# Optimization experiments

Measured on AMD Instinct MI355X. Metric: run time of the kernel, lower is better.

## Reference

```python
import jax, jax.numpy as jnp
import numpy as np
from jax import lax

# ---- static config (matches init_kwargs) ----
B, CIN, COUT, WDIM = 16, 256, 3, 512
IN_SIZE, SR, IMG = 128, 128, 256
UP = IMG // SR                      # 2
CLAMP = 256.0
PAD_SIZE = (SR - IN_SIZE) * UP // 2  # 0


def _design_lowpass_filter(numtaps, cutoff, width, fs):
    """numpy reimplementation of scipy.signal.firwin (kaiser window, pass_zero)."""
    nyq = fs / 2.0
    # kaiser_atten / kaiser_beta
    atten = 2.285 * (numtaps - 1) * np.pi * (width / nyq) + 7.95
    if atten > 50:
        beta = 0.1102 * (atten - 8.7)
    elif atten > 21:
        beta = 0.5842 * (atten - 21) ** 0.4 + 0.07886 * (atten - 21)
    else:
        beta = 0.0
    m = np.arange(numtaps) - (numtaps - 1) / 2.0
    c = cutoff / nyq
    h = c * np.sinc(c * m)          # ideal lowpass
    h *= np.kaiser(numtaps, beta)   # kaiser window
    h /= h.sum()                    # unity DC gain (pass_zero scaling)
    return h.astype(np.float32)


def _upsample2d(x, f, up):
    """Faithful upfirdn2d.upsample2d: zero-insert upsample + separable FIR, gain=up^2."""
    C = x.shape[1]
    fw = f.shape[0]
    f = f * (up * up) ** 0.5        # sqrt(gain) per separable pass
    f = f[::-1]                     # flip (torch conv2d is correlation on flipped f)
    p0 = (fw + up - 1) // 2
    p1 = (fw - up) // 2 + (up - 1)  # +up-1: trailing zeros from zero-insertion
    dn = ('NCHW', 'OIHW', 'NCHW')
    kx = jnp.tile(f.reshape(1, 1, 1, fw), (C, 1, 1, 1))
    x = lax.conv_general_dilated(x, kx, window_strides=(1, 1),
                                 padding=((0, 0), (p0, p1)), lhs_dilation=(1, up),
                                 dimension_numbers=dn, feature_group_count=C)
    ky = jnp.tile(f.reshape(1, 1, fw, 1), (C, 1, 1, 1))
    x = lax.conv_general_dilated(x, ky, window_strides=(1, 1),
                                 padding=((p0, p1), (0, 0)), lhs_dilation=(up, 1),
                                 dimension_numbers=dn, feature_group_count=C)
    return x


def setup_inputs() -> dict:
    key = jax.random.key(0)
    k1, k2, k3, k4, k5 = jax.random.split(key, 5)
    up_filter = jnp.asarray(_design_lowpass_filter(
        numtaps=6 * UP + 1, cutoff=SR * 2 ** (-0.9), width=SR - SR * 2 ** (-0.9), fs=IMG))
    return {
        'x': jax.random.normal(k1, (B, CIN, IN_SIZE, IN_SIZE), jnp.float32),
        'w': jax.random.normal(k2, (B, WDIM), jnp.float32),
        'affine_weight': jax.random.normal(k3, (CIN, WDIM), jnp.float32),
        'affine_bias': jnp.ones((CIN,), jnp.float32),
        'conv_weight': jax.random.normal(k4, (COUT, CIN, 1, 1), jnp.float32),
        'conv_bias': jax.random.normal(k5, (COUT,), jnp.float32) * 0.1,
        'up_filter': up_filter,
    }


def reference(x, w, affine_weight, affine_bias, conv_weight, conv_bias, up_filter):
    # affine: FullyConnectedLayer (linear, weight_gain = 1/sqrt(w_dim)), then * 1/sqrt(in_ch*k^2)
    styles = (w @ (affine_weight.T * (1.0 / np.sqrt(WDIM))) + affine_bias) * (1.0 / np.sqrt(CIN))
    # modulated 1x1 grouped conv (demodulate=False): out[b,o] = sum_i W[o,i]*s[b,i]*x[b,i]
    k = conv_weight[:, :, 0, 0]                       # [COUT, CIN]
    y = jnp.einsum('bihw,oi,bi->bohw', x, k, styles)  # [B, COUT, H, W]
    # bias_act: bias + clamp
    y = jnp.clip(y + conv_bias.reshape(1, -1, 1, 1), -CLAMP, CLAMP)
    # FIR upsample (up_factor != 1) + pad (pad_size == 0 here)
    y = _upsample2d(y, up_filter, UP)
    if PAD_SIZE:
        y = jnp.pad(y, ((0, 0), (0, 0), (PAD_SIZE, PAD_SIZE), (PAD_SIZE, PAD_SIZE)))
    return y  # [B, COUT, IMG, IMG]
```

## Files before the change

kernel.cpp:

```cpp
#include <hip/hip_runtime.h>
#include <hip/hip_bf16.h>

#define B_    16
#define CIN_  256
#define COUT_ 3
#define WDIM_ 512
#define H_    128
#define HW_   (H_*H_)
#define OH_   256

__global__ __launch_bounds__(64) void k_styles(const float* __restrict__ w,
    const float* __restrict__ aw, const float* __restrict__ ab,
    const float* __restrict__ cw, float* __restrict__ mw)
{
    int bi = blockIdx.x;
    int b = bi >> 8, i = bi & 255;
    int lane = threadIdx.x;
    const float* wr = w + b * WDIM_;
    const float* ar = aw + (size_t)i * WDIM_;
    float s = 0.f;
    #pragma unroll
    for (int t = 0; t < 8; ++t) s += wr[lane + 64*t] * ar[lane + 64*t];
    #pragma unroll
    for (int off = 32; off > 0; off >>= 1) s += __shfl_down(s, off);
    if (lane == 0) {
        float st = (s * 0.04419417382415922f + ab[i]) * 0.0625f;
        float4 v;
        v.x = cw[i]          * st;
        v.y = cw[CIN_ + i]   * st;
        v.z = cw[2*CIN_ + i] * st;
        v.w = 0.f;
        reinterpret_cast<float4*>(mw)[bi] = v;
    }
}

__global__ __launch_bounds__(256) void k_conv(const float* __restrict__ x,
    const float* __restrict__ mw, const float* __restrict__ cb,
    float* __restrict__ y)
{
    int b    = blockIdx.x >> 5;
    int base = ((blockIdx.x & 31) << 9) + (threadIdx.x << 1);
    const float2* xp  = reinterpret_cast<const float2*>(x + (size_t)b * CIN_ * HW_ + base);
    const float4* mwp = reinterpret_cast<const float4*>(mw) + b * CIN_;
    float a0x=0.f,a0y=0.f,a1x=0.f,a1y=0.f,a2x=0.f,a2y=0.f;
    #pragma unroll 8
    for (int i = 0; i < CIN_; ++i) {
        float2 xv = xp[(size_t)i * (HW_/2)];
        float4 m  = mwp[i];
        a0x += xv.x*m.x; a0y += xv.y*m.x;
        a1x += xv.x*m.y; a1y += xv.y*m.y;
        a2x += xv.x*m.z; a2y += xv.y*m.z;
    }
    float b0 = cb[0], b1 = cb[1], b2 = cb[2];
    auto cl = [](float v){ return fminf(fmaxf(v, -256.f), 256.f); };
    float* yp = y + (size_t)b * COUT_ * HW_ + base;
    *reinterpret_cast<float2*>(yp)          = make_float2(cl(a0x+b0), cl(a0y+b0));
    *reinterpret_cast<float2*>(yp +   HW_)  = make_float2(cl(a1x+b1), cl(a1y+b1));
    *reinterpret_cast<float2*>(yp + 2*HW_)  = make_float2(cl(a2x+b2), cl(a2y+b2));
}

__global__ __launch_bounds__(256) void k_upx(const float* __restrict__ y,
    const float* __restrict__ f, float* __restrict__ t)
{
    int idx = blockIdx.x * 256 + threadIdx.x;
    int q   = idx & 127;
    int row = idx >> 7;
    const float* yr = y + (size_t)row * H_;
    int i0 = q - 3;
    float v[7];
    #pragma unroll
    for (int j = 0; j < 7; ++j) {
        int i = i0 + j;
        v[j] = (i >= 0 && i < H_) ? yr[i] : 0.f;
    }
    float e = 0.f, o = 0.f;
    #pragma unroll
    for (int j = 0; j < 6; ++j) e += v[j] * f[11 - 2*j];
    #pragma unroll
    for (int j = 0; j < 7; ++j) o += v[j] * f[12 - 2*j];
    reinterpret_cast<float2*>(t + (size_t)row * OH_)[q] = make_float2(e * 2.f, o * 2.f);
}

__global__ __launch_bounds__(256) void k_upy(const float* __restrict__ t,
    const float* __restrict__ f, float* __restrict__ out)
{
    int idx  = blockIdx.x * 256 + threadIdx.x;
    int qx   = idx & 127;
    int rest = idx >> 7;
    int qy   = rest & 127;
    int p    = rest >> 7;
    const float2* tc = reinterpret_cast<const float2*>(t + (size_t)p * H_ * OH_) + qx;
    int i0 = qy - 3;
    float2 v[7];
    #pragma unroll
    for (int j = 0; j < 7; ++j) {
        int i = i0 + j;
        v[j] = (i >= 0 && i < H_) ? tc[(size_t)i * (OH_/2)] : make_float2(0.f, 0.f);
    }
    float r0c0=0.f, r0c1=0.f, r1c0=0.f, r1c1=0.f;
    #pragma unroll
    for (int j = 0; j < 6; ++j) { float c = f[11-2*j]; r0c0 += v[j].x*c; r0c1 += v[j].y*c; }
    #pragma unroll
    for (int j = 0; j < 7; ++j) { float c = f[12-2*j]; r1c0 += v[j].x*c; r1c1 += v[j].y*c; }
    size_t rowbase = ((size_t)p * OH_ + 2*qy) * OH_ + 2*qx;
    *reinterpret_cast<float2*>(out + rowbase)       = make_float2(r0c0 * 2.f, r0c1 * 2.f);
    *reinterpret_cast<float2*>(out + rowbase + OH_) = make_float2(r1c0 * 2.f, r1c1 * 2.f);
}

extern "C" void kernel_launch(void* const* d_in, const int* in_sizes, int n_in,
                              void* d_out, int out_size, void* d_ws, size_t ws_size,
                              hipStream_t stream)
{
    const float* x  = (const float*)d_in[0];
    const float* w  = (const float*)d_in[1];
    const float* aw = (const float*)d_in[2];
    const float* ab = (const float*)d_in[3];
    const float* cw = (const float*)d_in[4];
    const float* cb = (const float*)d_in[5];
    const float* f  = (const float*)d_in[6];

    float* mw = (float*)d_ws;
    float* y  = mw + B_ * CIN_ * 4;
    float* t  = y + (size_t)B_ * COUT_ * HW_;
    float* out = (float*)d_out;

    hipLaunchKernelGGL(k_styles, dim3(B_*CIN_), dim3(64),  0, stream, w, aw, ab, cw, mw);
    hipLaunchKernelGGL(k_conv,   dim3(B_*32),   dim3(256), 0, stream, x, mw, cb, y);
    hipLaunchKernelGGL(k_upx,    dim3(3072),    dim3(256), 0, stream, y, f, t);
    hipLaunchKernelGGL(k_upy,    dim3(3072),    dim3(256), 0, stream, t, f, out);
}
```

Before: 382.8 us.

## Fuse separable FIR upsample passes via shared-memory tiles and widen conv loads

The horizontal and vertical upsample passes become one kernel. It stages a 22x136 band of the low-res image in shared memory and computes both FIR passes in registers, so the intermediate buffer is never written to or read back from global memory. The conv kernel now handles four pixels per thread with float4 loads, which halves its block count to 256. The risks are lower occupancy and parallelism: the fused upsample launches only 384 blocks, the conv only 256, and the horizontal FIR work is recomputed across overlapping rows.

```diff
diff --git a/kernel.cpp b/kernel.cpp
--- a/kernel.cpp
+++ b/kernel.cpp
@@ -38,73 +38,91 @@
     const float* __restrict__ mw, const float* __restrict__ cb,
     float* __restrict__ y)
 {
-    int b    = blockIdx.x >> 5;
-    int base = ((blockIdx.x & 31) << 9) + (threadIdx.x << 1);
-    const float2* xp  = reinterpret_cast<const float2*>(x + (size_t)b * CIN_ * HW_ + base);
+    int b    = blockIdx.x >> 4;
+    int base = ((blockIdx.x & 15) << 10) + (threadIdx.x << 2);
+    const float4* xp  = reinterpret_cast<const float4*>(x + (size_t)b * CIN_ * HW_ + base);
     const float4* mwp = reinterpret_cast<const float4*>(mw) + b * CIN_;
-    float a0x=0.f,a0y=0.f,a1x=0.f,a1y=0.f,a2x=0.f,a2y=0.f;
+    float a0[4] = {0,0,0,0}, a1[4] = {0,0,0,0}, a2[4] = {0,0,0,0};
     #pragma unroll 8
     for (int i = 0; i < CIN_; ++i) {
-        float2 xv = xp[(size_t)i * (HW_/2)];
+        float4 xv = xp[(size_t)i * (HW_/4)];
         float4 m  = mwp[i];
-        a0x += xv.x*m.x; a0y += xv.y*m.x;
-        a1x += xv.x*m.y; a1y += xv.y*m.y;
-        a2x += xv.x*m.z; a2y += xv.y*m.z;
+        float xs[4] = { xv.x, xv.y, xv.z, xv.w };
+        #pragma unroll
+        for (int p = 0; p < 4; ++p) {
+            a0[p] += xs[p]*m.x;
+            a1[p] += xs[p]*m.y;
+            a2[p] += xs[p]*m.z;
+        }
     }
     float b0 = cb[0], b1 = cb[1], b2 = cb[2];
     auto cl = [](float v){ return fminf(fmaxf(v, -256.f), 256.f); };
     float* yp = y + (size_t)b * COUT_ * HW_ + base;
-    *reinterpret_cast<float2*>(yp)          = make_float2(cl(a0x+b0), cl(a0y+b0));
-    *reinterpret_cast<float2*>(yp +   HW_)  = make_float2(cl(a1x+b1), cl(a1y+b1));
-    *reinterpret_cast<float2*>(yp + 2*HW_)  = make_float2(cl(a2x+b2), cl(a2y+b2));
+    float4 o0, o1, o2;
+    o0.x=cl(a0[0]+b0); o0.y=cl(a0[1]+b0); o0.z=cl(a0[2]+b0); o0.w=cl(a0[3]+b0);
+    o1.x=cl(a1[0]+b1); o1.y=cl(a1[1]+b1); o1.z=cl(a1[2]+b1); o1.w=cl(a1[3]+b1);
+    o2.x=cl(a2[0]+b2); o2.y=cl(a2[1]+b2); o2.z=cl(a2[2]+b2); o2.w=cl(a2[3]+b2);
+    *reinterpret_cast<float4*>(yp)          = o0;
+    *reinterpret_cast<float4*>(yp +   HW_)  = o1;
+    *reinterpret_cast<float4*>(yp + 2*HW_)  = o2;
 }
 
-__global__ __launch_bounds__(256) void k_upx(const float* __restrict__ y,
-    const float* __restrict__ f, float* __restrict__ t)
-{
-    int idx = blockIdx.x * 256 + threadIdx.x;
-    int q   = idx & 127;
-    int row = idx >> 7;
-    const float* yr = y + (size_t)row * H_;
-    int i0 = q - 3;
-    float v[7];
-    #pragma unroll
-    for (int j = 0; j < 7; ++j) {
-        int i = i0 + j;
-        v[j] = (i >= 0 && i < H_) ? yr[i] : 0.f;
-    }
-    float e = 0.f, o = 0.f;
-    #pragma unroll
-    for (int j = 0; j < 6; ++j) e += v[j] * f[11 - 2*j];
-    #pragma unroll
-    for (int j = 0; j < 7; ++j) o += v[j] * f[12 - 2*j];
-    reinterpret_cast<float2*>(t + (size_t)row * OH_)[q] = make_float2(e * 2.f, o * 2.f);
-}
-
-__global__ __launch_bounds__(256) void k_upy(const float* __restrict__ t,
+#define BAND_  16
+#define LROWS_ 22
+#define LCOLS_ 136
+__global__ __launch_bounds__(256) void k_up(const float* __restrict__ y,
     const float* __restrict__ f, float* __restrict__ out)
 {
-    int idx  = blockIdx.x * 256 + threadIdx.x;
-    int qx   = idx & 127;
-    int rest = idx >> 7;
-    int qy   = rest & 127;
-    int p    = rest >> 7;
-    const float2* tc = reinterpret_cast<const float2*>(t + (size_t)p * H_ * OH_) + qx;
-    int i0 = qy - 3;
-    float2 v[7];
+    __shared__ float ys[LROWS_][LCOLS_];
+    int p    = blockIdx.x >> 3;
+    int q0   = (blockIdx.x & 7) * BAND_;
+    int tid  = threadIdx.x;
+
+    const float* yp = y + (size_t)p * HW_;
+    for (int e = tid; e < LROWS_ * LCOLS_; e += 256) {
+        int r = e / LCOLS_, c = e - r * LCOLS_;
+        int gr = q0 - 3 + r, gc = c - 3;
+        float v = 0.f;
+        if (gr >= 0 && gr < H_ && gc >= 0 && gc < H_) v = yp[gr * H_ + gc];
+        ys[r][c] = v;
+    }
+    __syncthreads();
+
+    float fe[6], fo[7];
     #pragma unroll
-    for (int j = 0; j < 7; ++j) {
-        int i = i0 + j;
-        v[j] = (i >= 0 && i < H_) ? tc[(size_t)i * (OH_/2)] : make_float2(0.f, 0.f);
+    for (int i = 0; i < 6; ++i) fe[i] = f[11 - 2*i];
+    #pragma unroll
+    for (int i = 0; i < 7; ++i) fo[i] = f[12 - 2*i];
+
+    int qx  = tid & 127;
+    int qy0 = tid >> 7;
+    float* outp = out + (size_t)p * OH_ * OH_;
+
+    #pragma unroll
+    for (int k = 0; k < 8; ++k) {
+        int qy = qy0 + 2*k;
+        float e_[7], o_[7];
+        #pragma unroll
+        for (int j = 0; j < 7; ++j) {
+            const float* row = &ys[qy + j][qx];
+            float e = 0.f, o = 0.f;
+            #pragma unroll
+            for (int i = 0; i < 6; ++i) e += row[i] * fe[i];
+            #pragma unroll
+            for (int i = 0; i < 7; ++i) o += row[i] * fo[i];
+            e_[j] = e; o_[j] = o;
+        }
+        float r0e=0.f, r0o=0.f, r1e=0.f, r1o=0.f;
+        #pragma unroll
+        for (int j = 0; j < 6; ++j) { r0e += fe[j]*e_[j]; r0o += fe[j]*o_[j]; }
+        #pragma unroll
+        for (int j = 0; j < 7; ++j) { r1e += fo[j]*e_[j]; r1o += fo[j]*o_[j]; }
+        int oy = 2*(q0 + qy);
+        float2* d0 = reinterpret_cast<float2*>(outp + (size_t)oy * OH_) + qx;
+        float2* d1 = reinterpret_cast<float2*>(outp + (size_t)(oy+1) * OH_) + qx;
+        *d0 = make_float2(r0e * 4.f, r0o * 4.f);
+        *d1 = make_float2(r1e * 4.f, r1o * 4.f);
     }
-    float r0c0=0.f, r0c1=0.f, r1c0=0.f, r1c1=0.f;
-    #pragma unroll
-    for (int j = 0; j < 6; ++j) { float c = f[11-2*j]; r0c0 += v[j].x*c; r0c1 += v[j].y*c; }
-    #pragma unroll
-    for (int j = 0; j < 7; ++j) { float c = f[12-2*j]; r1c0 += v[j].x*c; r1c1 += v[j].y*c; }
-    size_t rowbase = ((size_t)p * OH_ + 2*qy) * OH_ + 2*qx;
-    *reinterpret_cast<float2*>(out + rowbase)       = make_float2(r0c0 * 2.f, r0c1 * 2.f);
-    *reinterpret_cast<float2*>(out + rowbase + OH_) = make_float2(r1c0 * 2.f, r1c1 * 2.f);
 }
 
 extern "C" void kernel_launch(void* const* d_in, const int* in_sizes, int n_in,
@@ -121,11 +139,9 @@
 
     float* mw = (float*)d_ws;
     float* y  = mw + B_ * CIN_ * 4;
-    float* t  = y + (size_t)B_ * COUT_ * HW_;
     float* out = (float*)d_out;
 
     hipLaunchKernelGGL(k_styles, dim3(B_*CIN_), dim3(64),  0, stream, w, aw, ab, cw, mw);
-    hipLaunchKernelGGL(k_conv,   dim3(B_*32),   dim3(256), 0, stream, x, mw, cb, y);
-    hipLaunchKernelGGL(k_upx,    dim3(3072),    dim3(256), 0, stream, y, f, t);
-    hipLaunchKernelGGL(k_upy,    dim3(3072),    dim3(256), 0, stream, t, f, out);
+    hipLaunchKernelGGL(k_conv,   dim3(B_*16),   dim3(256), 0, stream, x, mw, cb, y);
+    hipLaunchKernelGGL(k_up,     dim3(48*8),    dim3(256), 0, stream, y, f, out);
 }
```

Result: no change. 379.0 us (-1.0%).
